# Optimization experiments

Hardware: AMD Instinct MI355X
Metric: run time of the kernel (lower is better)

## Reference

```python
import jax, jax.numpy as jnp
import numpy as np
from jax import lax

H = 64
X = 128
T = 8192
A_SCALE = 0.1
A_IDENTITY = 0.9


def setup_inputs() -> dict:
    key = jax.random.key(0)
    k1, k2, k3, k4 = jax.random.split(key, 4)
    x_seq = jax.random.normal(k1, (T, X), dtype=jnp.float32)
    h0 = jax.random.normal(k2, (H,), dtype=jnp.float32)
    # orthogonal-ish init for A_raw (exact orthogonality not required for correctness)
    A_raw = jnp.linalg.qr(jax.random.normal(k3, (H, H), dtype=jnp.float32))[0]
    B = jax.random.normal(k4, (H, X), dtype=jnp.float32) * (1.0 / np.sqrt(X))
    c = jnp.zeros((H,), dtype=jnp.float32)
    return {"x_seq": x_seq, "h0": h0, "A_raw": A_raw, "B": B, "c": c}


def reference(x_seq, h0, A_raw, B, c):
    # A = a_identity * I + a_scale * A_raw  (fixed dense transition matrix)
    A = A_IDENTITY * jnp.eye(H, dtype=x_seq.dtype) + A_SCALE * A_raw
    # b_t = B x_t + c, kept as column vectors [T, H, 1]
    b_seq = (x_seq @ B.T + c[None, :])[..., None]
    A_seq = jnp.broadcast_to(A, (T, H, H))

    def combine(left, right):
        A1, b1 = left
        A2, b2 = right
        return (A2 @ A1, A2 @ b1 + b2)

    A_pref, b_pref = lax.associative_scan(combine, (A_seq, b_seq), axis=0)
    b_pref = b_pref[..., 0]                 # [T, H]
    h_all = A_pref @ h0 + b_pref            # [T, H]
    return h_all
```

## Files before the change

kernel.cpp:

```cpp
#include <hip/hip_runtime.h>
#include <hip/hip_bf16.h>

#define T_ 8192
#define H_ 64
#define X_ 128
#define C_ 128
#define L_ 64
#define K1_TB 16

__device__ __forceinline__ float bcast(float v, int src) {
    return __int_as_float(__builtin_amdgcn_readlane(__float_as_int(v), src));
}

__device__ __forceinline__ float lru_step(const float* arow, float h, float b_i) {
    float a0 = b_i, a1 = 0.f, a2 = 0.f, a3 = 0.f;
#pragma unroll
    for (int j = 0; j < 16; ++j) {
        a0 = fmaf(arow[j],      bcast(h, j),      a0);
        a1 = fmaf(arow[j + 16], bcast(h, j + 16), a1);
        a2 = fmaf(arow[j + 32], bcast(h, j + 32), a2);
        a3 = fmaf(arow[j + 48], bcast(h, j + 48), a3);
    }
    return (a0 + a1) + (a2 + a3);
}

__device__ __forceinline__ void pin_row(float* arow) {
#pragma unroll
    for (int q = 0; q < 64; ++q) asm volatile("" : "+v"(arow[q]));
}

__device__ __forceinline__ void load_arow_A(const float* __restrict__ A_raw,
                                            int lane, float* arow) {
    const float4* a4 = (const float4*)(A_raw + lane * H_);
#pragma unroll
    for (int q = 0; q < 16; ++q) {
        float4 t4 = a4[q];
        arow[4 * q + 0] = 0.1f * t4.x;
        arow[4 * q + 1] = 0.1f * t4.y;
        arow[4 * q + 2] = 0.1f * t4.z;
        arow[4 * q + 3] = 0.1f * t4.w;
    }
#pragma unroll
    for (int q = 0; q < 64; ++q) arow[q] += (q == lane) ? 0.9f : 0.0f;
    pin_row(arow);
}

__device__ __forceinline__ void load_row(const float* __restrict__ M,
                                         int lane, float* arow) {
    const float4* a4 = (const float4*)(M + lane * H_);
#pragma unroll
    for (int q = 0; q < 16; ++q) {
        float4 t4 = a4[q];
        arow[4 * q + 0] = t4.x;
        arow[4 * q + 1] = t4.y;
        arow[4 * q + 2] = t4.z;
        arow[4 * q + 3] = t4.w;
    }
    pin_row(arow);
}

#define PSTR 68
__global__ __launch_bounds__(256) void k_bproj_pow(
        const float* __restrict__ x, const float* __restrict__ A_raw,
        const float* __restrict__ B, const float* __restrict__ c,
        float* __restrict__ bws, float* __restrict__ A2g,
        float* __restrict__ A4g, float* __restrict__ A8g) {
    __shared__ float M1[H_ * PSTR];
    __shared__ float M2[H_ * PSTR];
    const int tid = threadIdx.x;

    if (blockIdx.x < T_ / K1_TB) {
        const int lane = tid & 63;
        const int w    = __builtin_amdgcn_readfirstlane(tid >> 6);
        const int t0   = blockIdx.x * K1_TB + w * 4;
        const float cc = c[lane];
        float acc[4];
#pragma unroll
        for (int r = 0; r < 4; ++r) acc[r] = cc;
        const float* Brow = B + lane * X_;
#pragma unroll
        for (int kc = 0; kc < 4; ++kc) {
            float4 br[8];
            const float4* b4 = (const float4*)(Brow + kc * 32);
#pragma unroll
            for (int q = 0; q < 8; ++q) br[q] = b4[q];
#pragma unroll
            for (int r = 0; r < 4; ++r) {
                const float4* xr = (const float4*)(x + (size_t)(t0 + r) * X_ + kc * 32);
#pragma unroll
                for (int q = 0; q < 8; ++q) {
                    float4 xv = xr[q];
                    acc[r] = fmaf(br[q].x, xv.x, acc[r]);
                    acc[r] = fmaf(br[q].y, xv.y, acc[r]);
                    acc[r] = fmaf(br[q].z, xv.z, acc[r]);
                    acc[r] = fmaf(br[q].w, xv.w, acc[r]);
                }
            }
        }
#pragma unroll
        for (int r = 0; r < 4; ++r) bws[(size_t)(t0 + r) * H_ + lane] = acc[r];
        return;
    }

    for (int idx = tid; idx < H_ * H_; idx += 256) {
        const int r = idx >> 6, cc = idx & 63;
        M1[r * PSTR + cc] = 0.1f * A_raw[idx] + ((r == cc) ? 0.9f : 0.0f);
    }
    __syncthreads();

    const int r = tid >> 2;
    const int q = tid & 3;
    const int c0 = q * 16;

    {
        float acc[16];
#pragma unroll
        for (int j = 0; j < 16; ++j) acc[j] = 0.f;
        for (int k = 0; k < H_; ++k) {
            const float m1 = M1[r * PSTR + k];
            const float4* s2 = (const float4*)&M1[k * PSTR + c0];
#pragma unroll
            for (int j4 = 0; j4 < 4; ++j4) {
                float4 bv = s2[j4];
                acc[4 * j4 + 0] = fmaf(m1, bv.x, acc[4 * j4 + 0]);
                acc[4 * j4 + 1] = fmaf(m1, bv.y, acc[4 * j4 + 1]);
                acc[4 * j4 + 2] = fmaf(m1, bv.z, acc[4 * j4 + 2]);
                acc[4 * j4 + 3] = fmaf(m1, bv.w, acc[4 * j4 + 3]);
            }
        }
#pragma unroll
        for (int j = 0; j < 16; ++j) {
            M2[r * PSTR + c0 + j] = acc[j];
            A2g[r * H_ + c0 + j]  = acc[j];
        }
    }
    __syncthreads();
    {
        float acc[16];
#pragma unroll
        for (int j = 0; j < 16; ++j) acc[j] = 0.f;
        for (int k = 0; k < H_; ++k) {
            const float m1 = M2[r * PSTR + k];
            const float4* s2 = (const float4*)&M2[k * PSTR + c0];
#pragma unroll
            for (int j4 = 0; j4 < 4; ++j4) {
                float4 bv = s2[j4];
                acc[4 * j4 + 0] = fmaf(m1, bv.x, acc[4 * j4 + 0]);
                acc[4 * j4 + 1] = fmaf(m1, bv.y, acc[4 * j4 + 1]);
                acc[4 * j4 + 2] = fmaf(m1, bv.z, acc[4 * j4 + 2]);
                acc[4 * j4 + 3] = fmaf(m1, bv.w, acc[4 * j4 + 3]);
            }
        }
        __syncthreads();
#pragma unroll
        for (int j = 0; j < 16; ++j) {
            M1[r * PSTR + c0 + j] = acc[j];
            A4g[r * H_ + c0 + j]  = acc[j];
        }
    }
    __syncthreads();
    {
        float acc[16];
#pragma unroll
        for (int j = 0; j < 16; ++j) acc[j] = 0.f;
        for (int k = 0; k < H_; ++k) {
            const float m1 = M1[r * PSTR + k];
            const float4* s2 = (const float4*)&M1[k * PSTR + c0];
#pragma unroll
            for (int j4 = 0; j4 < 4; ++j4) {
                float4 bv = s2[j4];
                acc[4 * j4 + 0] = fmaf(m1, bv.x, acc[4 * j4 + 0]);
                acc[4 * j4 + 1] = fmaf(m1, bv.y, acc[4 * j4 + 1]);
                acc[4 * j4 + 2] = fmaf(m1, bv.z, acc[4 * j4 + 2]);
                acc[4 * j4 + 3] = fmaf(m1, bv.w, acc[4 * j4 + 3]);
            }
        }
#pragma unroll
        for (int j = 0; j < 16; ++j) A8g[r * H_ + c0 + j] = acc[j];
    }
}

#define KB_ROWS 23
__global__ __launch_bounds__(256) void k_btilde(
        const float* __restrict__ A_raw, const float* __restrict__ A2,
        const float* __restrict__ A4, const float* __restrict__ bsrc,
        float* __restrict__ bt8) {
    __shared__ __align__(16) float buf[2][KB_ROWS][H_];
    const int tid = threadIdx.x, lane = tid & 63, w = tid >> 6;
    const int t0 = blockIdx.x * K1_TB;

    for (int idx = tid; idx < KB_ROWS * H_; idx += 256) {
        const int row = idx >> 6, hh = idx & 63;
        const int t = t0 - 7 + row;
        buf[0][row][hh] = (t >= 0) ? bsrc[(size_t)t * H_ + hh] : 0.f;
    }
    __syncthreads();

    int src = 0;
    float arow[64];
#pragma unroll
    for (int pass = 0; pass < 3; ++pass) {
        const int dist = 1 << pass;
        if (pass == 0)      load_arow_A(A_raw, lane, arow);
        else if (pass == 1) load_row(A2, lane, arow);
        else                load_row(A4, lane, arow);
        for (int row = w; row < KB_ROWS; row += 4) {
            const int t = t0 - 7 + row;
            float val = buf[src][row][lane];
            if (row >= dist && t >= 0 && (t & 63) >= dist) {
                const float4* h4 = (const float4*)buf[src][row - dist];
                float a0 = val, a1 = 0.f, a2 = 0.f, a3 = 0.f;
#pragma unroll
                for (int qq = 0; qq < 16; ++qq) {
                    float4 hv = h4[qq];
                    a0 = fmaf(arow[4 * qq + 0], hv.x, a0);
                    a1 = fmaf(arow[4 * qq + 1], hv.y, a1);
                    a2 = fmaf(arow[4 * qq + 2], hv.z, a2);
                    a3 = fmaf(arow[4 * qq + 3], hv.w, a3);
                }
                val = (a0 + a1) + (a2 + a3);
            }
            buf[src ^ 1][row][lane] = val;
        }
        __syncthreads();
        src ^= 1;
    }
    for (int r2 = w; r2 < 16; r2 += 4) {
        bt8[(size_t)(t0 + r2) * H_ + lane] = buf[src][7 + r2][lane];
    }
}

__global__ __launch_bounds__(64) void k_phase1(
        const float* __restrict__ A8, const float* __restrict__ bt8,
        float* __restrict__ v, float* __restrict__ ALQ) {
    const int lane = threadIdx.x, bid = blockIdx.x;
    float arow[64];
    load_row(A8, lane, arow);
    if (bid < C_) {
        const float* bc = bt8 + (size_t)bid * L_ * H_;
        float y = bc[7 * H_ + lane];
#pragma unroll
        for (int k = 1; k <= 7; ++k)
            y = lru_step(arow, y, bc[(size_t)(7 + 8 * k) * H_ + lane]);
        v[bid * H_ + lane] = y;
    } else {
        const int col = bid - C_;
        float y = (lane == col) ? 1.f : 0.f;
#pragma unroll
        for (int k = 0; k < 8; ++k) y = lru_step(arow, y, 0.f);
        ALQ[lane * H_ + col] = y;
    }
}

__global__ __launch_bounds__(64) void k_prep2(
        const float* __restrict__ ALQ, const float* __restrict__ v,
        float* __restrict__ Q8, float* __restrict__ vt) {
    const int lane = threadIdx.x, bid = blockIdx.x;
    float arow[64];
    load_row(ALQ, lane, arow);
    if (bid < H_) {
        const int col = bid;
        float y = ALQ[lane * H_ + col];
#pragma unroll
        for (int k = 0; k < 7; ++k) y = lru_step(arow, y, 0.f);
        Q8[lane * H_ + col] = y;
    } else {
        const int c = bid - H_ + 8;
        float y = v[(c - 8) * H_ + lane];
#pragma unroll
        for (int k = 7; k >= 1; --k)
            y = lru_step(arow, y, v[(c - k) * H_ + lane]);
        vt[c * H_ + lane] = y;
    }
}

__global__ __launch_bounds__(256) void k_phase2(
        const float* __restrict__ ALQ, const float* __restrict__ Q8,
        const float* __restrict__ h0, const float* __restrict__ v,
        const float* __restrict__ vt, float* __restrict__ hstart) {
    __shared__ __align__(16) float s8[8][H_];
    const int tid = threadIdx.x, lane = tid & 63, w = tid >> 6;
    float arow8[64];
    load_row(Q8, lane, arow8);
    if (w == 0) {
        float arowQ[64];
        load_row(ALQ, lane, arowQ);
        float s = h0[lane];
        hstart[lane] = s;
        s8[0][lane]  = s;
#pragma unroll
        for (int cc = 0; cc < 7; ++cc) {
            s = lru_step(arowQ, s, v[cc * H_ + lane]);
            hstart[(cc + 1) * H_ + lane] = s;
            s8[cc + 1][lane] = s;
        }
    }
    __syncthreads();
    const int r0 = w, r1 = w + 4;
    float y0 = s8[r0][lane], y1 = s8[r1][lane];
#pragma unroll
    for (int k = 1; k <= 15; ++k) {
        const int c0 = r0 + 8 * k, c1 = r1 + 8 * k;
        y0 = lru_step(arow8, y0, vt[c0 * H_ + lane]);
        y1 = lru_step(arow8, y1, vt[c1 * H_ + lane]);
        hstart[c0 * H_ + lane] = y0;
        hstart[c1 * H_ + lane] = y1;
    }
}

__global__ __launch_bounds__(256) void k_phase3(
        const float* __restrict__ A_raw, const float* __restrict__ A8,
        const float* __restrict__ hstart, const float* __restrict__ bws,
        const float* __restrict__ bt8, float* __restrict__ out) {
    __shared__ __align__(16) float h8[8][H_];
    const int tid = threadIdx.x, lane = tid & 63, w = tid >> 6;
    const int cid = blockIdx.x;
    float arow8[64];
    load_row(A8, lane, arow8);
    float* oc = out + (size_t)cid * L_ * H_;
    if (w == 0) {
        float arowA[64];
        load_arow_A(A_raw, lane, arowA);
        float y = hstart[cid * H_ + lane];
#pragma unroll
        for (int i = 0; i < 8; ++i) {
            y = lru_step(arowA, y, bws[((size_t)cid * L_ + i) * H_ + lane]);
            oc[(size_t)i * H_ + lane] = y;
            h8[i][lane] = y;
        }
    }
    __syncthreads();
    const int r0 = w, r1 = w + 4;
    float y0 = h8[r0][lane], y1 = h8[r1][lane];
#pragma unroll
    for (int k = 1; k <= 7; ++k) {
        const int i0 = r0 + 8 * k, i1 = r1 + 8 * k;
        y0 = lru_step(arow8, y0, bt8[((size_t)cid * L_ + i0) * H_ + lane]);
        y1 = lru_step(arow8, y1, bt8[((size_t)cid * L_ + i1) * H_ + lane]);
        oc[(size_t)i0 * H_ + lane] = y0;
        oc[(size_t)i1 * H_ + lane] = y1;
    }
}

extern "C" void kernel_launch(void* const* d_in, const int* in_sizes, int n_in,
                              void* d_out, int out_size, void* d_ws, size_t ws_size,
                              hipStream_t stream) {
    const float* x     = (const float*)d_in[0];
    const float* h0    = (const float*)d_in[1];
    const float* A_raw = (const float*)d_in[2];
    const float* B     = (const float*)d_in[3];
    const float* c     = (const float*)d_in[4];
    float* out = (float*)d_out;
    float* ws  = (float*)d_ws;

    float* bws    = ws;
    float* bt8    = bws + T_ * H_;
    float* A2     = bt8 + T_ * H_;
    float* A4     = A2 + H_ * H_;
    float* A8     = A4 + H_ * H_;
    float* ALQ    = A8 + H_ * H_;
    float* Q8     = ALQ + H_ * H_;
    float* v      = Q8 + H_ * H_;
    float* vt     = v + C_ * H_;
    float* hstart = vt + C_ * H_;

    k_bproj_pow<<<T_ / K1_TB + 1, 256, 0, stream>>>(x, A_raw, B, c, bws, A2, A4, A8);
    k_btilde  <<<T_ / K1_TB,     256, 0, stream>>>(A_raw, A2, A4, bws, bt8);
    k_phase1  <<<C_ + H_,        64,  0, stream>>>(A8, bt8, v, ALQ);
    k_prep2   <<<H_ + (C_ - 8),  64,  0, stream>>>(ALQ, v, Q8, vt);
    k_phase2  <<<1,              256, 0, stream>>>(ALQ, Q8, h0, v, vt, hstart);
    k_phase3  <<<C_,             256, 0, stream>>>(A_raw, A8, hstart, bws, bt8, out);
}
```

Measured before the change: 82.41 us.

## Fuse six kernel launches into one persistent kernel with atomic grid barriers

```diff
diff --git a/kernel.cpp b/kernel.cpp
--- a/kernel.cpp
+++ b/kernel.cpp
@@ -6,7 +6,19 @@
 #define X_ 128
 #define C_ 128
 #define L_ 64
-#define K1_TB 16
+#define NB 512
+#define MS 68
+
+#define OFF_BT8 (T_ * H_)
+#define OFF_A2  (2 * T_ * H_)
+#define OFF_A4  (OFF_A2 + 4096)
+#define OFF_A8  (OFF_A4 + 4096)
+#define OFF_Q   (OFF_A8 + 4096)
+#define OFF_Q8  (OFF_Q + 4096)
+#define OFF_V   (OFF_Q8 + 4096)
+#define OFF_VT  (OFF_V + C_ * H_)
+#define OFF_HS  (OFF_VT + C_ * H_)
+#define OFF_CNT (OFF_HS + C_ * H_)
 
 __device__ __forceinline__ float bcast(float v, int src) {
     return __int_as_float(__builtin_amdgcn_readlane(__float_as_int(v), src));
@@ -59,286 +71,278 @@
     pin_row(arow);
 }
 
-#define PSTR 68
-__global__ __launch_bounds__(256) void k_bproj_pow(
-        const float* __restrict__ x, const float* __restrict__ A_raw,
-        const float* __restrict__ B, const float* __restrict__ c,
-        float* __restrict__ bws, float* __restrict__ A2g,
-        float* __restrict__ A4g, float* __restrict__ A8g) {
-    __shared__ float M1[H_ * PSTR];
-    __shared__ float M2[H_ * PSTR];
+__device__ __forceinline__ void gsync(unsigned* cnt, int phase) {
+    __syncthreads();
+    if (threadIdx.x == 0) {
+        __threadfence();
+        __hip_atomic_fetch_add(&cnt[phase], 1u, __ATOMIC_ACQ_REL,
+                               __HIP_MEMORY_SCOPE_AGENT);
+        while (__hip_atomic_load(&cnt[phase], __ATOMIC_RELAXED,
+                                 __HIP_MEMORY_SCOPE_AGENT) < (unsigned)NB)
+            __builtin_amdgcn_s_sleep(2);
+        __threadfence();
+    }
+    __syncthreads();
+}
+
+__device__ __forceinline__ void sq64(const float* Min, float* Mout, float* gout) {
     const int tid = threadIdx.x;
-
-    if (blockIdx.x < T_ / K1_TB) {
-        const int lane = tid & 63;
-        const int w    = __builtin_amdgcn_readfirstlane(tid >> 6);
-        const int t0   = blockIdx.x * K1_TB + w * 4;
-        const float cc = c[lane];
-        float acc[4];
-#pragma unroll
-        for (int r = 0; r < 4; ++r) acc[r] = cc;
-        const float* Brow = B + lane * X_;
-#pragma unroll
-        for (int kc = 0; kc < 4; ++kc) {
-            float4 br[8];
-            const float4* b4 = (const float4*)(Brow + kc * 32);
-#pragma unroll
-            for (int q = 0; q < 8; ++q) br[q] = b4[q];
-#pragma unroll
-            for (int r = 0; r < 4; ++r) {
-                const float4* xr = (const float4*)(x + (size_t)(t0 + r) * X_ + kc * 32);
-#pragma unroll
-                for (int q = 0; q < 8; ++q) {
-                    float4 xv = xr[q];
-                    acc[r] = fmaf(br[q].x, xv.x, acc[r]);
-                    acc[r] = fmaf(br[q].y, xv.y, acc[r]);
-                    acc[r] = fmaf(br[q].z, xv.z, acc[r]);
-                    acc[r] = fmaf(br[q].w, xv.w, acc[r]);
+    const int r = tid >> 2, c0 = (tid & 3) * 16;
+    float acc[16];
+#pragma unroll
+    for (int j = 0; j < 16; ++j) acc[j] = 0.f;
+    for (int k = 0; k < H_; ++k) {
+        const float a = Min[r * MS + k];
+        const float4* b4 = (const float4*)(Min + k * MS + c0);
+#pragma unroll
+        for (int j4 = 0; j4 < 4; ++j4) {
+            float4 bv = b4[j4];
+            acc[4 * j4 + 0] = fmaf(a, bv.x, acc[4 * j4 + 0]);
+            acc[4 * j4 + 1] = fmaf(a, bv.y, acc[4 * j4 + 1]);
+            acc[4 * j4 + 2] = fmaf(a, bv.z, acc[4 * j4 + 2]);
+            acc[4 * j4 + 3] = fmaf(a, bv.w, acc[4 * j4 + 3]);
+        }
+    }
+#pragma unroll
+    for (int j = 0; j < 16; ++j) Mout[r * MS + c0 + j] = acc[j];
+    if (gout) {
+#pragma unroll
+        for (int j = 0; j < 16; ++j) gout[r * H_ + c0 + j] = acc[j];
+    }
+    __syncthreads();
+}
+
+__device__ __forceinline__ void bproj_rows4(const float* __restrict__ x,
+                                            const float* __restrict__ B,
+                                            const float* __restrict__ c,
+                                            float* __restrict__ bws,
+                                            int t0, int lane) {
+    const float cc = c[lane];
+    float acc[4] = {cc, cc, cc, cc};
+    const float* Brow = B + lane * X_;
+#pragma unroll
+    for (int kc = 0; kc < 4; ++kc) {
+        float4 br[8];
+        const float4* b4 = (const float4*)(Brow + kc * 32);
+#pragma unroll
+        for (int q = 0; q < 8; ++q) br[q] = b4[q];
+#pragma unroll
+        for (int r = 0; r < 4; ++r) {
+            const float4* xr = (const float4*)(x + (size_t)(t0 + r) * X_ + kc * 32);
+#pragma unroll
+            for (int q = 0; q < 8; ++q) {
+                float4 xv = xr[q];
+                acc[r] = fmaf(br[q].x, xv.x, acc[r]);
+                acc[r] = fmaf(br[q].y, xv.y, acc[r]);
+                acc[r] = fmaf(br[q].z, xv.z, acc[r]);
+                acc[r] = fmaf(br[q].w, xv.w, acc[r]);
+            }
+        }
+    }
+#pragma unroll
+    for (int r = 0; r < 4; ++r) bws[(size_t)(t0 + r) * H_ + lane] = acc[r];
+}
+
+__device__ __forceinline__ void bproj_row1(const float* __restrict__ x,
+                                           const float* __restrict__ B,
+                                           const float* __restrict__ c,
+                                           float* __restrict__ bws,
+                                           int t, int lane) {
+    float acc = c[lane];
+    const float4* Br = (const float4*)(B + lane * X_);
+    const float4* xr = (const float4*)(x + (size_t)t * X_);
+#pragma unroll
+    for (int q = 0; q < 32; ++q) {
+        float4 bv = Br[q];
+        float4 xv = xr[q];
+        acc = fmaf(bv.x, xv.x, acc);
+        acc = fmaf(bv.y, xv.y, acc);
+        acc = fmaf(bv.z, xv.z, acc);
+        acc = fmaf(bv.w, xv.w, acc);
+    }
+    bws[(size_t)t * H_ + lane] = acc;
+}
+
+#define KB_ROWS 39
+
+__global__ __launch_bounds__(256, 2) void lru_mega(
+        const float* __restrict__ x, const float* __restrict__ h0,
+        const float* __restrict__ A_raw, const float* __restrict__ B,
+        const float* __restrict__ c, float* __restrict__ out,
+        float* __restrict__ ws, unsigned* __restrict__ cnt) {
+    __shared__ __align__(16) float smem[2 * H_ * MS];
+    float* M1 = smem;
+    float* M2 = smem + H_ * MS;
+
+    const int tid = threadIdx.x, lane = tid & 63, w = tid >> 6;
+    const int b = blockIdx.x;
+
+    float* bws    = ws;
+    float* bt8    = ws + OFF_BT8;
+    float* A2g    = ws + OFF_A2;
+    float* A4g    = ws + OFF_A4;
+    float* A8g    = ws + OFF_A8;
+    float* Qg     = ws + OFF_Q;
+    float* Q8g    = ws + OFF_Q8;
+    float* v      = ws + OFF_V;
+    float* vt     = ws + OFF_VT;
+    float* hstart = ws + OFF_HS;
+
+    if (b < 511) {
+        bproj_rows4(x, B, c, bws, b * 16 + w * 4, lane);
+        if (b < 16 && w == 0) bproj_row1(x, B, c, bws, 8176 + b, lane);
+    } else {
+        for (int idx = tid; idx < H_ * H_; idx += 256) {
+            const int r = idx >> 6, cc2 = idx & 63;
+            M1[r * MS + cc2] = 0.1f * A_raw[idx] + ((r == cc2) ? 0.9f : 0.0f);
+        }
+        __syncthreads();
+        sq64(M1, M2, A2g);
+        sq64(M2, M1, A4g);
+    }
+    gsync(cnt, 0);
+
+    if (b < 256) {
+        float* buf0 = smem;
+        float* buf1 = smem + KB_ROWS * H_;
+        const int t0 = b * 32;
+        for (int idx = tid; idx < KB_ROWS * H_; idx += 256) {
+            const int row = idx >> 6;
+            const int t = t0 - 7 + row;
+            buf0[idx] = (t >= 0) ? bws[(size_t)t * H_ + (idx & 63)] : 0.f;
+        }
+        __syncthreads();
+        float* srcb = buf0; float* dstb = buf1;
+        float arow[64];
+#pragma unroll
+        for (int pass = 0; pass < 3; ++pass) {
+            const int dist = 1 << pass;
+            if (pass == 0)      load_arow_A(A_raw, lane, arow);
+            else if (pass == 1) load_row(A2g, lane, arow);
+            else                load_row(A4g, lane, arow);
+            for (int row = w; row < KB_ROWS; row += 4) {
+                const int t = t0 - 7 + row;
+                float val = srcb[row * H_ + lane];
+                if (row >= dist && t >= 0 && (t & 63) >= dist) {
+                    const float4* h4 = (const float4*)(srcb + (row - dist) * H_);
+                    float a0 = val, a1 = 0.f, a2 = 0.f, a3 = 0.f;
+#pragma unroll
+                    for (int qq = 0; qq < 16; ++qq) {
+                        float4 hv = h4[qq];
+                        a0 = fmaf(arow[4 * qq + 0], hv.x, a0);
+                        a1 = fmaf(arow[4 * qq + 1], hv.y, a1);
+                        a2 = fmaf(arow[4 * qq + 2], hv.z, a2);
+                        a3 = fmaf(arow[4 * qq + 3], hv.w, a3);
+                    }
+                    val = (a0 + a1) + (a2 + a3);
                 }
+                dstb[row * H_ + lane] = val;
             }
-        }
-#pragma unroll
-        for (int r = 0; r < 4; ++r) bws[(size_t)(t0 + r) * H_ + lane] = acc[r];
-        return;
-    }
-
-    for (int idx = tid; idx < H_ * H_; idx += 256) {
-        const int r = idx >> 6, cc = idx & 63;
-        M1[r * PSTR + cc] = 0.1f * A_raw[idx] + ((r == cc) ? 0.9f : 0.0f);
-    }
-    __syncthreads();
-
-    const int r = tid >> 2;
-    const int q = tid & 3;
-    const int c0 = q * 16;
+            __syncthreads();
+            float* tmp = srcb; srcb = dstb; dstb = tmp;
+        }
+        for (int r2 = w; r2 < 32; r2 += 4)
+            bt8[(size_t)(t0 + r2) * H_ + lane] = srcb[(7 + r2) * H_ + lane];
+    } else if (b == 511) {
+        sq64(M1, M2, A8g);
+        sq64(M2, M1, nullptr);
+        sq64(M1, M2, nullptr);
+        sq64(M2, M1, Qg);
+    }
+    gsync(cnt, 1);
 
     {
-        float acc[16];
-#pragma unroll
-        for (int j = 0; j < 16; ++j) acc[j] = 0.f;
-        for (int k = 0; k < H_; ++k) {
-            const float m1 = M1[r * PSTR + k];
-            const float4* s2 = (const float4*)&M1[k * PSTR + c0];
-#pragma unroll
-            for (int j4 = 0; j4 < 4; ++j4) {
-                float4 bv = s2[j4];
-                acc[4 * j4 + 0] = fmaf(m1, bv.x, acc[4 * j4 + 0]);
-                acc[4 * j4 + 1] = fmaf(m1, bv.y, acc[4 * j4 + 1]);
-                acc[4 * j4 + 2] = fmaf(m1, bv.z, acc[4 * j4 + 2]);
-                acc[4 * j4 + 3] = fmaf(m1, bv.w, acc[4 * j4 + 3]);
+        const int gw = b * 4 + w;
+        if (gw < C_) {
+            float arow[64];
+            load_row(A8g, lane, arow);
+            const float* bc = bt8 + (size_t)gw * L_ * H_;
+            float y = bc[7 * H_ + lane];
+#pragma unroll
+            for (int k = 1; k <= 7; ++k)
+                y = lru_step(arow, y, bc[(size_t)(7 + 8 * k) * H_ + lane]);
+            v[gw * H_ + lane] = y;
+        } else if (b == 511) {
+            sq64(M1, M2, nullptr);
+            sq64(M2, M1, nullptr);
+            sq64(M1, M2, Q8g);
+        }
+    }
+    gsync(cnt, 2);
+
+    {
+        const int gw = b * 4 + w;
+        if (gw < C_ - 8) {
+            const int cc2 = gw + 8;
+            float arow[64];
+            load_row(Qg, lane, arow);
+            float y = v[(cc2 - 8) * H_ + lane];
+#pragma unroll
+            for (int k = 7; k >= 1; --k)
+                y = lru_step(arow, y, v[(cc2 - k) * H_ + lane]);
+            vt[cc2 * H_ + lane] = y;
+        }
+    }
+    gsync(cnt, 3);
+
+    if (b == 0) {
+        float* s8 = smem;
+        float arow8[64];
+        load_row(Q8g, lane, arow8);
+        if (w == 0) {
+            float arowQ[64];
+            load_row(Qg, lane, arowQ);
+            float s = h0[lane];
+            hstart[lane] = s;
+            s8[lane] = s;
+#pragma unroll
+            for (int cc2 = 0; cc2 < 7; ++cc2) {
+                s = lru_step(arowQ, s, v[cc2 * H_ + lane]);
+                hstart[(cc2 + 1) * H_ + lane] = s;
+                s8[(cc2 + 1) * H_ + lane] = s;
             }
         }
-#pragma unroll
-        for (int j = 0; j < 16; ++j) {
-            M2[r * PSTR + c0 + j] = acc[j];
-            A2g[r * H_ + c0 + j]  = acc[j];
-        }
-    }
-    __syncthreads();
-    {
-        float acc[16];
-#pragma unroll
-        for (int j = 0; j < 16; ++j) acc[j] = 0.f;
-        for (int k = 0; k < H_; ++k) {
-            const float m1 = M2[r * PSTR + k];
-            const float4* s2 = (const float4*)&M2[k * PSTR + c0];
-#pragma unroll
-            for (int j4 = 0; j4 < 4; ++j4) {
-                float4 bv = s2[j4];
-                acc[4 * j4 + 0] = fmaf(m1, bv.x, acc[4 * j4 + 0]);
-                acc[4 * j4 + 1] = fmaf(m1, bv.y, acc[4 * j4 + 1]);
-                acc[4 * j4 + 2] = fmaf(m1, bv.z, acc[4 * j4 + 2]);
-                acc[4 * j4 + 3] = fmaf(m1, bv.w, acc[4 * j4 + 3]);
+        __syncthreads();
+        const int r0 = w, r1 = w + 4;
+        float y0 = s8[r0 * H_ + lane], y1 = s8[r1 * H_ + lane];
+#pragma unroll
+        for (int k = 1; k <= 15; ++k) {
+            const int c0 = r0 + 8 * k, c1 = r1 + 8 * k;
+            y0 = lru_step(arow8, y0, vt[c0 * H_ + lane]);
+            y1 = lru_step(arow8, y1, vt[c1 * H_ + lane]);
+            hstart[c0 * H_ + lane] = y0;
+            hstart[c1 * H_ + lane] = y1;
+        }
+    }
+    gsync(cnt, 4);
+
+    if (b < C_) {
+        float* h8 = smem;
+        float arow8[64];
+        load_row(A8g, lane, arow8);
+        float* oc = out + (size_t)b * L_ * H_;
+        if (w == 0) {
+            float arowA[64];
+            load_arow_A(A_raw, lane, arowA);
+            float y = hstart[b * H_ + lane];
+#pragma unroll
+            for (int i = 0; i < 8; ++i) {
+                y = lru_step(arowA, y, bws[((size_t)b * L_ + i) * H_ + lane]);
+                oc[(size_t)i * H_ + lane] = y;
+                h8[i * H_ + lane] = y;
             }
         }
         __syncthreads();
-#pragma unroll
-        for (int j = 0; j < 16; ++j) {
-            M1[r * PSTR + c0 + j] = acc[j];
-            A4g[r * H_ + c0 + j]  = acc[j];
-        }
-    }
-    __syncthreads();
-    {
-        float acc[16];
-#pragma unroll
-        for (int j = 0; j < 16; ++j) acc[j] = 0.f;
-        for (int k = 0; k < H_; ++k) {
-            const float m1 = M1[r * PSTR + k];
-            const float4* s2 = (const float4*)&M1[k * PSTR + c0];
-#pragma unroll
-            for (int j4 = 0; j4 < 4; ++j4) {
-                float4 bv = s2[j4];
-                acc[4 * j4 + 0] = fmaf(m1, bv.x, acc[4 * j4 + 0]);
-                acc[4 * j4 + 1] = fmaf(m1, bv.y, acc[4 * j4 + 1]);
-                acc[4 * j4 + 2] = fmaf(m1, bv.z, acc[4 * j4 + 2]);
-                acc[4 * j4 + 3] = fmaf(m1, bv.w, acc[4 * j4 + 3]);
-            }
-        }
-#pragma unroll
-        for (int j = 0; j < 16; ++j) A8g[r * H_ + c0 + j] = acc[j];
-    }
-}
-
-#define KB_ROWS 23
-__global__ __launch_bounds__(256) void k_btilde(
-        const float* __restrict__ A_raw, const float* __restrict__ A2,
-        const float* __restrict__ A4, const float* __restrict__ bsrc,
-        float* __restrict__ bt8) {
-    __shared__ __align__(16) float buf[2][KB_ROWS][H_];
-    const int tid = threadIdx.x, lane = tid & 63, w = tid >> 6;
-    const int t0 = blockIdx.x * K1_TB;
-
-    for (int idx = tid; idx < KB_ROWS * H_; idx += 256) {
-        const int row = idx >> 6, hh = idx & 63;
-        const int t = t0 - 7 + row;
-        buf[0][row][hh] = (t >= 0) ? bsrc[(size_t)t * H_ + hh] : 0.f;
-    }
-    __syncthreads();
-
-    int src = 0;
-    float arow[64];
-#pragma unroll
-    for (int pass = 0; pass < 3; ++pass) {
-        const int dist = 1 << pass;
-        if (pass == 0)      load_arow_A(A_raw, lane, arow);
-        else if (pass == 1) load_row(A2, lane, arow);
-        else                load_row(A4, lane, arow);
-        for (int row = w; row < KB_ROWS; row += 4) {
-            const int t = t0 - 7 + row;
-            float val = buf[src][row][lane];
-            if (row >= dist && t >= 0 && (t & 63) >= dist) {
-                const float4* h4 = (const float4*)buf[src][row - dist];
-                float a0 = val, a1 = 0.f, a2 = 0.f, a3 = 0.f;
-#pragma unroll
-                for (int qq = 0; qq < 16; ++qq) {
-                    float4 hv = h4[qq];
-                    a0 = fmaf(arow[4 * qq + 0], hv.x, a0);
-                    a1 = fmaf(arow[4 * qq + 1], hv.y, a1);
-                    a2 = fmaf(arow[4 * qq + 2], hv.z, a2);
-                    a3 = fmaf(arow[4 * qq + 3], hv.w, a3);
-                }
-                val = (a0 + a1) + (a2 + a3);
-            }
-            buf[src ^ 1][row][lane] = val;
-        }
-        __syncthreads();
-        src ^= 1;
-    }
-    for (int r2 = w; r2 < 16; r2 += 4) {
-        bt8[(size_t)(t0 + r2) * H_ + lane] = buf[src][7 + r2][lane];
-    }
-}
-
-__global__ __launch_bounds__(64) void k_phase1(
-        const float* __restrict__ A8, const float* __restrict__ bt8,
-        float* __restrict__ v, float* __restrict__ ALQ) {
-    const int lane = threadIdx.x, bid = blockIdx.x;
-    float arow[64];
-    load_row(A8, lane, arow);
-    if (bid < C_) {
-        const float* bc = bt8 + (size_t)bid * L_ * H_;
-        float y = bc[7 * H_ + lane];
-#pragma unroll
-        for (int k = 1; k <= 7; ++k)
-            y = lru_step(arow, y, bc[(size_t)(7 + 8 * k) * H_ + lane]);
-        v[bid * H_ + lane] = y;
-    } else {
-        const int col = bid - C_;
-        float y = (lane == col) ? 1.f : 0.f;
-#pragma unroll
-        for (int k = 0; k < 8; ++k) y = lru_step(arow, y, 0.f);
-        ALQ[lane * H_ + col] = y;
-    }
-}
-
-__global__ __launch_bounds__(64) void k_prep2(
-        const float* __restrict__ ALQ, const float* __restrict__ v,
-        float* __restrict__ Q8, float* __restrict__ vt) {
-    const int lane = threadIdx.x, bid = blockIdx.x;
-    float arow[64];
-    load_row(ALQ, lane, arow);
-    if (bid < H_) {
-        const int col = bid;
-        float y = ALQ[lane * H_ + col];
-#pragma unroll
-        for (int k = 0; k < 7; ++k) y = lru_step(arow, y, 0.f);
-        Q8[lane * H_ + col] = y;
-    } else {
-        const int c = bid - H_ + 8;
-        float y = v[(c - 8) * H_ + lane];
-#pragma unroll
-        for (int k = 7; k >= 1; --k)
-            y = lru_step(arow, y, v[(c - k) * H_ + lane]);
-        vt[c * H_ + lane] = y;
-    }
-}
-
-__global__ __launch_bounds__(256) void k_phase2(
-        const float* __restrict__ ALQ, const float* __restrict__ Q8,
-        const float* __restrict__ h0, const float* __restrict__ v,
-        const float* __restrict__ vt, float* __restrict__ hstart) {
-    __shared__ __align__(16) float s8[8][H_];
-    const int tid = threadIdx.x, lane = tid & 63, w = tid >> 6;
-    float arow8[64];
-    load_row(Q8, lane, arow8);
-    if (w == 0) {
-        float arowQ[64];
-        load_row(ALQ, lane, arowQ);
-        float s = h0[lane];
-        hstart[lane] = s;
-        s8[0][lane]  = s;
-#pragma unroll
-        for (int cc = 0; cc < 7; ++cc) {
-            s = lru_step(arowQ, s, v[cc * H_ + lane]);
-            hstart[(cc + 1) * H_ + lane] = s;
-            s8[cc + 1][lane] = s;
-        }
-    }
-    __syncthreads();
-    const int r0 = w, r1 = w + 4;
-    float y0 = s8[r0][lane], y1 = s8[r1][lane];
-#pragma unroll
-    for (int k = 1; k <= 15; ++k) {
-        const int c0 = r0 + 8 * k, c1 = r1 + 8 * k;
-        y0 = lru_step(arow8, y0, vt[c0 * H_ + lane]);
-        y1 = lru_step(arow8, y1, vt[c1 * H_ + lane]);
-        hstart[c0 * H_ + lane] = y0;
-        hstart[c1 * H_ + lane] = y1;
-    }
-}
-
-__global__ __launch_bounds__(256) void k_phase3(
-        const float* __restrict__ A_raw, const float* __restrict__ A8,
-        const float* __restrict__ hstart, const float* __restrict__ bws,
-        const float* __restrict__ bt8, float* __restrict__ out) {
-    __shared__ __align__(16) float h8[8][H_];
-    const int tid = threadIdx.x, lane = tid & 63, w = tid >> 6;
-    const int cid = blockIdx.x;
-    float arow8[64];
-    load_row(A8, lane, arow8);
-    float* oc = out + (size_t)cid * L_ * H_;
-    if (w == 0) {
-        float arowA[64];
-        load_arow_A(A_raw, lane, arowA);
-        float y = hstart[cid * H_ + lane];
-#pragma unroll
-        for (int i = 0; i < 8; ++i) {
-            y = lru_step(arowA, y, bws[((size_t)cid * L_ + i) * H_ + lane]);
-            oc[(size_t)i * H_ + lane] = y;
-            h8[i][lane] = y;
-        }
-    }
-    __syncthreads();
-    const int r0 = w, r1 = w + 4;
-    float y0 = h8[r0][lane], y1 = h8[r1][lane];
-#pragma unroll
-    for (int k = 1; k <= 7; ++k) {
-        const int i0 = r0 + 8 * k, i1 = r1 + 8 * k;
-        y0 = lru_step(arow8, y0, bt8[((size_t)cid * L_ + i0) * H_ + lane]);
-        y1 = lru_step(arow8, y1, bt8[((size_t)cid * L_ + i1) * H_ + lane]);
-        oc[(size_t)i0 * H_ + lane] = y0;
-        oc[(size_t)i1 * H_ + lane] = y1;
+        const int r0 = w, r1 = w + 4;
+        float y0 = h8[r0 * H_ + lane], y1 = h8[r1 * H_ + lane];
+#pragma unroll
+        for (int k = 1; k <= 7; ++k) {
+            const int i0 = r0 + 8 * k, i1 = r1 + 8 * k;
+            y0 = lru_step(arow8, y0, bt8[((size_t)b * L_ + i0) * H_ + lane]);
+            y1 = lru_step(arow8, y1, bt8[((size_t)b * L_ + i1) * H_ + lane]);
+            oc[(size_t)i0 * H_ + lane] = y0;
+            oc[(size_t)i1 * H_ + lane] = y1;
+        }
     }
 }
 
@@ -352,22 +356,8 @@
     const float* c     = (const float*)d_in[4];
     float* out = (float*)d_out;
     float* ws  = (float*)d_ws;
-
-    float* bws    = ws;
-    float* bt8    = bws + T_ * H_;
-    float* A2     = bt8 + T_ * H_;
-    float* A4     = A2 + H_ * H_;
-    float* A8     = A4 + H_ * H_;
-    float* ALQ    = A8 + H_ * H_;
-    float* Q8     = ALQ + H_ * H_;
-    float* v      = Q8 + H_ * H_;
-    float* vt     = v + C_ * H_;
-    float* hstart = vt + C_ * H_;
-
-    k_bproj_pow<<<T_ / K1_TB + 1, 256, 0, stream>>>(x, A_raw, B, c, bws, A2, A4, A8);
-    k_btilde  <<<T_ / K1_TB,     256, 0, stream>>>(A_raw, A2, A4, bws, bt8);
-    k_phase1  <<<C_ + H_,        64,  0, stream>>>(A8, bt8, v, ALQ);
-    k_prep2   <<<H_ + (C_ - 8),  64,  0, stream>>>(ALQ, v, Q8, vt);
-    k_phase2  <<<1,              256, 0, stream>>>(ALQ, Q8, h0, v, vt, hstart);
-    k_phase3  <<<C_,             256, 0, stream>>>(A_raw, A8, hstart, bws, bt8, out);
-}
+    unsigned* cnt = (unsigned*)(ws + OFF_CNT);
+
+    hipMemsetAsync(cnt, 0, 64, stream);
+    lru_mega<<<NB, 256, 0, stream>>>(x, h0, A_raw, B, c, out, ws, cnt);
+}
```

Result: slower. 270.1 us (+227.7%).
